# Optimization experiments

Measured on AMD Instinct MI355X. Metric: run time of the kernel, lower is better.

Reference implementation:

```python
import jax, jax.numpy as jnp
import numpy as np

S = 64        # state_dim
M = 16        # message_dim
H = 128       # hidden_unit_message_dim
HR = 128      # hidden_unit_readout_dim
NSTEPS = 10
N_NODES = 10000
N_FACTORS = 40000


def setup_inputs() -> dict:
    rng = np.random.default_rng(0)
    n, F = N_NODES, N_FACTORS
    # random undirected factor pairs (u, v) with u < v
    u = rng.integers(0, n - 1, F)
    v = rng.integers(u + 1, n)
    # var->factor directed edges: (u, i) and (v, i) for factor i
    v2f_src = np.stack([u, v], 1).ravel().astype(np.int32)          # [E]
    v2f_dst = np.repeat(np.arange(F), 2).astype(np.int32)           # [E]
    b = rng.normal(size=n).astype(np.float32)
    Juv = rng.normal(size=F).astype(np.float32)
    Jvu = rng.normal(size=F).astype(np.float32)
    feat_u = np.stack([b[u], b[v], Juv, Jvu], 1)
    feat_v = np.stack([b[v], b[u], Juv, Jvu], 1)
    feat = np.stack([feat_u, feat_v], 1).reshape(-1, 4).astype(np.float32)  # [E,4]
    p = lambda *s: (0.1 * rng.normal(size=s)).astype(np.float32)
    z = lambda *s: np.zeros(s, np.float32)
    inp = {
        'v2f_src': jnp.asarray(v2f_src), 'v2f_dst': jnp.asarray(v2f_dst),
        'f2v_src': jnp.asarray(v2f_dst), 'f2v_dst': jnp.asarray(v2f_src),
        'feat_v2f': jnp.asarray(feat), 'feat_f2v': jnp.asarray(feat),
        'n_nodes': n, 'n_factors': F,
        'Qw': jnp.asarray(p(4, M * M)), 'Qb': jnp.asarray(z(M * M)),
        'mp1_w1': jnp.asarray(p(2 * S, H)), 'mp1_b1': jnp.asarray(z(H)),
        'mp1_w2': jnp.asarray(p(H, H)), 'mp1_b2': jnp.asarray(z(H)),
        'mp1_w3': jnp.asarray(p(H, M)), 'mp1_b3': jnp.asarray(z(M)),
        'mp2_w1': jnp.asarray(p(2 * S, H)), 'mp2_b1': jnp.asarray(z(H)),
        'mp2_w2': jnp.asarray(p(H, H)), 'mp2_b2': jnp.asarray(z(H)),
        'mp2_w3': jnp.asarray(p(H, M)), 'mp2_b3': jnp.asarray(z(M)),
        'g1_wih': jnp.asarray(p(M, 3 * S)), 'g1_whh': jnp.asarray(p(S, 3 * S)),
        'g1_bih': jnp.asarray(z(3 * S)), 'g1_bhh': jnp.asarray(z(3 * S)),
        'g2_wih': jnp.asarray(p(M, 3 * S)), 'g2_whh': jnp.asarray(p(S, 3 * S)),
        'g2_bih': jnp.asarray(z(3 * S)), 'g2_bhh': jnp.asarray(z(3 * S)),
        'ro_w1': jnp.asarray(p(S, HR)), 'ro_b1': jnp.asarray(z(HR)),
        'ro_w2': jnp.asarray(p(HR, HR)), 'ro_b2': jnp.asarray(z(HR)),
        'ro_w3': jnp.asarray(p(HR, 2)), 'ro_b3': jnp.asarray(z(2)),
    }
    return inp


def _mlp(x, w1, b1, w2, b2, w3, b3):
    h = jax.nn.relu(x @ w1 + b1)
    h = jax.nn.relu(h @ w2 + b2)
    return h @ w3 + b3


def _gru(x, h, wih, whh, bih, bhh):
    # torch.nn.GRUCell gate order: r, z, n
    gi = x @ wih + bih
    gh = h @ whh + bhh
    ir, iz, inn = jnp.split(gi, 3, axis=-1)
    hr, hz, hn = jnp.split(gh, 3, axis=-1)
    r = jax.nn.sigmoid(ir + hr)
    zg = jax.nn.sigmoid(iz + hz)
    ng = jnp.tanh(inn + r * hn)
    return (1.0 - zg) * ng + zg * h


def reference(v2f_src, v2f_dst, f2v_src, f2v_dst, feat_v2f, feat_f2v,
              n_nodes, n_factors, Qw, Qb,
              mp1_w1, mp1_b1, mp1_w2, mp1_b2, mp1_w3, mp1_b3,
              mp2_w1, mp2_b1, mp2_w2, mp2_b2, mp2_w3, mp2_b3,
              g1_wih, g1_whh, g1_bih, g1_bhh,
              g2_wih, g2_whh, g2_bih, g2_bhh,
              ro_w1, ro_b1, ro_w2, ro_b2, ro_w3, ro_b3):
    var_h = jnp.zeros((n_nodes, S), feat_v2f.dtype)
    fac_h = jnp.zeros((n_factors, S), feat_v2f.dtype)
    # per-edge transform matrices are the same every step; hoist out of the loop
    q1 = (feat_v2f @ Qw + Qb).reshape(-1, M, M)  # [E, M, M]
    q2 = (feat_f2v @ Qw + Qb).reshape(-1, M, M)
    for _ in range(NSTEPS):
        # var -> factor
        x = jnp.concatenate([var_h[v2f_src], fac_h[v2f_dst]], axis=-1)  # [E, 2S]
        m = _mlp(x, mp1_w1, mp1_b1, mp1_w2, mp1_b2, mp1_w3, mp1_b3)    # [E, M]
        m = jnp.einsum('eij,ej->ei', q1, m)
        fac_msg = jax.ops.segment_sum(m, v2f_dst, num_segments=n_factors)
        fac_h = _gru(fac_msg, fac_h, g1_wih, g1_whh, g1_bih, g1_bhh)
        # factor -> var
        x = jnp.concatenate([fac_h[f2v_src], var_h[f2v_dst]], axis=-1)
        m = _mlp(x, mp2_w1, mp2_b1, mp2_w2, mp2_b2, mp2_w3, mp2_b3)
        m = jnp.einsum('eij,ej->ei', q2, m)
        var_msg = jax.ops.segment_sum(m, f2v_dst, num_segments=n_nodes)
        var_h = _gru(var_msg, var_h, g2_wih, g2_whh, g2_bih, g2_bhh)
    out = _mlp(var_h, ro_w1, ro_b1, ro_w2, ro_b2, ro_w3, ro_b3)  # [n_nodes, 2]
    return jax.nn.softmax(out, axis=1)
```

## Files before the change

### kernel.cpp

```cpp
#include <hip/hip_runtime.h>

#define NSTEPS 10

typedef __attribute__((ext_vector_type(8))) short bf16x8;
typedef __attribute__((ext_vector_type(4))) short bf16x4;
typedef __attribute__((ext_vector_type(4))) float f32x4;

__device__ __forceinline__ float sigmoidf_(float x) { return 1.0f / (1.0f + __expf(-x)); }
__device__ __forceinline__ float tanh_fast(float x) {
  const float e = __expf(2.f * x);
  return 1.f - 2.f / (e + 1.f);
}

__device__ __forceinline__ short bf16_(float x) {
  union { float f; unsigned u; } c; c.f = x;
  unsigned r = (c.u + 0x7FFFu + ((c.u >> 16) & 1u)) >> 16;
  return (short)r;
}
__device__ __forceinline__ unsigned pk2_(float a, float b) {
  union { float f; unsigned u; } ca, cb; ca.f = a; cb.f = b;
  return __builtin_amdgcn_perm(cb.u + 0x8000u, ca.u + 0x8000u, 0x07060302u);
}
__device__ __forceinline__ short pk1_(float a) {
  union { float f; unsigned u; } c; c.f = a;
  return (short)((c.u + 0x8000u) >> 16);
}
__device__ __forceinline__ float lo_(unsigned u) { union { unsigned u; float f; } c; c.u = u << 16; return c.f; }
__device__ __forceinline__ float hi_(unsigned u) { union { unsigned u; float f; } c; c.u = u & 0xffff0000u; return c.f; }

__device__ __forceinline__ f32x4 mfma_16x16x32(bf16x8 a, bf16x8 b, f32x4 c) {
  return __builtin_amdgcn_mfma_f32_16x16x32_bf16(a, b, c, 0, 0, 0);
}

struct PackJob { const float* src; int N; int KS; int nchunks; };
struct PackArgs {
  PackJob jb[10];
  const float* Qw; const float* Qb;
  const float* g1wih; const float* g1whh;
  const float* g2wih; const float* g2whh;
};

__global__ __launch_bounds__(256) void k_pack(PackArgs a, short* __restrict__ out, int total) {
  const int g = blockIdx.x * 256 + threadIdx.x;
  if (g >= total) return;
  int c = g >> 9;
  const int r = g & 511;
  const int j = r & 7, n = (r >> 3) & 15, q = (r >> 7) & 3;
  const int kq = q * 8 + j;
  float val = 0.f;
  bool done = false;
  #pragma unroll
  for (int ji = 0; ji < 10; ++ji) {
    if (!done && c < a.jb[ji].nchunks) {
      const int ks = c % a.jb[ji].KS;
      const int nt = c / a.jb[ji].KS;
      const int k = ks * 32 + kq;
      val = a.jb[ji].src[(size_t)k * a.jb[ji].N + nt * 16 + n];
      done = true;
    }
    if (!done) c -= a.jb[ji].nchunks;
  }
  if (!done) {
    if (c < 5) {
      val = 0.f;
      if (kq < 16) val = (c < 4) ? a.Qw[c * 256 + n * 16 + kq] : a.Qb[n * 16 + kq];
    } else {
      c -= 5;
      const float* wih = (c < 48) ? a.g1wih : a.g2wih;
      const float* whh = (c < 48) ? a.g1whh : a.g2whh;
      if (c >= 48) c -= 48;
      const int nt = c / 3, ks = c % 3;
      const int k = ks * 32 + kq;
      const int ng = nt * 16 + n;
      const int gate = ng >> 6, s = ng & 63;
      val = 0.f;
      if (gate == 0) {
        if (k < 16) val = wih[k * 192 + s];
        else if (k < 80) val = whh[(k - 16) * 192 + s];
      } else if (gate == 1) {
        if (k < 16) val = wih[k * 192 + 64 + s];
        else if (k < 80) val = whh[(k - 16) * 192 + 64 + s];
      } else if (gate == 2) {
        if (k < 16) val = wih[k * 192 + 128 + s];
      } else {
        if (k >= 16 && k < 80) val = whh[(k - 16) * 192 + 128 + s];
      }
    }
  }
  out[g] = bf16_(val);
}

__global__ __launch_bounds__(256) void k_dense2(
    const float* __restrict__ X0, const short* __restrict__ W0, short* __restrict__ C0,
    int rows0, int g0,
    const float* __restrict__ X1, const short* __restrict__ W1, short* __restrict__ C1,
    int rows1, float* __restrict__ zeroPtr,
    const float* __restrict__ gruMsg, float* __restrict__ gruH,
    const short* __restrict__ gruW,
    const float* __restrict__ gbih, const float* __restrict__ gbhh)
{
  constexpr int KS = 2, K = 64, STR = K + 8;
  __shared__ short Xs[64 * STR];
  __shared__ short SA[64 * 104];
  const int t = threadIdx.x, lane = t & 63, wave = t >> 6;
  const int m = lane & 15, quad = lane >> 4;

  const float* X; const short* Wf; short* C; int rows, rbase;
  const bool job0 = (int)blockIdx.x < g0;
  if (job0) {
    X = X0; Wf = W0; C = C0; rows = rows0; rbase = blockIdx.x * 64;
  } else {
    X = X1; Wf = W1; C = C1; rows = rows1; rbase = ((int)blockIdx.x - g0) * 64;
    if (zeroPtr) {
      const int zr = rbase + (t >> 2);
      if (zr < rows1) {
        f32x4 z = {0.f, 0.f, 0.f, 0.f};
        *(f32x4*)(zeroPtr + (size_t)zr * 16 + (t & 3) * 4) = z;
      }
    }
  }

  bf16x8 b[2][KS];
  #pragma unroll
  for (int nt2 = 0; nt2 < 2; ++nt2)
    #pragma unroll
    for (int ks = 0; ks < KS; ++ks)
      b[nt2][ks] = ((const bf16x8*)Wf)[((wave * 2 + nt2) * KS + ks) * 64 + lane];

  if (job0 && gruMsg) {
    {
      const int r = t >> 2, q4 = t & 3, rg = rbase + r;
      #pragma unroll
      for (int i = 0; i < 6; ++i) {
        const int c = q4 * 4 + i * 16;
        f32x4 v = {0.f, 0.f, 0.f, 0.f};
        if (rg < rows) {
          if (c < 16)      v = *(const f32x4*)(gruMsg + (size_t)rg * 16 + c);
          else if (c < 80) v = *(const f32x4*)(gruH + (size_t)rg * 64 + (c - 16));
        }
        *(unsigned*)&SA[r * 104 + c]     = pk2_(v.x, v.y);
        *(unsigned*)&SA[r * 104 + c + 2] = pk2_(v.z, v.w);
      }
    }
    __syncthreads();
    f32x4 acc[16] = {};
    #pragma unroll
    for (int ks = 0; ks < 3; ++ks) {
      const bf16x8 a = *(const bf16x8*)&SA[(wave * 16 + m) * 104 + ks * 32 + quad * 8];
      #pragma unroll
      for (int nt = 0; nt < 16; ++nt)
        acc[nt] = mfma_16x16x32(a, ((const bf16x8*)gruW)[(nt * 3 + ks) * 64 + lane], acc[nt]);
    }
    #pragma unroll
    for (int nt = 0; nt < 4; ++nt) {
      const int s = nt * 16 + m;
      const float br  = gbih[s] + gbhh[s];
      const float bz  = gbih[64 + s] + gbhh[64 + s];
      const float bin = gbih[128 + s];
      const float bhn = gbhh[128 + s];
      #pragma unroll
      for (int reg = 0; reg < 4; ++reg) {
        const int lr = wave * 16 + quad * 4 + reg;
        const int rg = rbase + lr;
        short hv = 0;
        if (rg < rows) {
          const float ho = gruH[(size_t)rg * 64 + s];
          const float rr = sigmoidf_(acc[nt][reg] + br);
          const float zz = sigmoidf_(acc[4 + nt][reg] + bz);
          const float nn = tanh_fast(acc[8 + nt][reg] + bin + rr * (acc[12 + nt][reg] + bhn));
          const float hn = (1.f - zz) * nn + zz * ho;
          gruH[(size_t)rg * 64 + s] = hn;
          hv = pk1_(hn);
        }
        Xs[lr * STR + s] = hv;
      }
    }
    __syncthreads();
  } else {
    const int r = t >> 2, q4 = t & 3, rg = rbase + r;
    #pragma unroll
    for (int i = 0; i < K / 16; ++i) {
      const int cc = q4 * 4 + i * 16;
      f32x4 v = {0.f, 0.f, 0.f, 0.f};
      if (rg < rows) v = *(const f32x4*)(X + (size_t)rg * K + cc);
      *(unsigned*)&Xs[r * STR + cc]     = pk2_(v.x, v.y);
      *(unsigned*)&Xs[r * STR + cc + 2] = pk2_(v.z, v.w);
    }
    __syncthreads();
  }

  f32x4 acc[2][4] = {};
  #pragma unroll
  for (int ks = 0; ks < KS; ++ks) {
    bf16x8 afr[4];
    #pragma unroll
    for (int mt = 0; mt < 4; ++mt)
      afr[mt] = *(const bf16x8*)&Xs[(mt * 16 + m) * STR + ks * 32 + quad * 8];
    #pragma unroll
    for (int nt2 = 0; nt2 < 2; ++nt2)
      #pragma unroll
      for (int mt = 0; mt < 4; ++mt)
        acc[nt2][mt] = mfma_16x16x32(afr[mt], b[nt2][ks], acc[nt2][mt]);
  }

  #pragma unroll
  for (int nt2 = 0; nt2 < 2; ++nt2) {
    const int col = (wave * 2 + nt2) * 16 + m;
    #pragma unroll
    for (int mt = 0; mt < 4; ++mt)
      #pragma unroll
      for (int rr = 0; rr < 4; ++rr) {
        const int rg = rbase + mt * 16 + quad * 4 + rr;
        if (rg < rows) C[(size_t)rg * 128 + col] = pk1_(acc[nt2][mt][rr]);
      }
  }
}

template<bool PAIRED>
__global__ __launch_bounds__(256) void k_edge(
    const short* __restrict__ Pa, const short* __restrict__ Pb,
    const int* __restrict__ src, const int* __restrict__ dst,
    const float* __restrict__ feat,
    const float* __restrict__ b1, const float* __restrict__ b2,
    const float* __restrict__ b3,
    const short* __restrict__ w2f, const short* __restrict__ w3f,
    const short* __restrict__ qf,
    float* __restrict__ outMsg,
    float* __restrict__ facH, const short* __restrict__ gruW,
    const float* __restrict__ gbih, const float* __restrict__ gbhh,
    int E, int F)
{
  __shared__ short h1s[64 * 136];
  __shared__ short ms[64 * 40];
  __shared__ short AsG[32 * 104];
  __shared__ float feats[64 * 4];
  __shared__ int sidx[64], didx[64];

  const int t = threadIdx.x, lane = t & 63, wave = t >> 6;
  const int e0 = blockIdx.x * 64;
  const int f0 = e0 >> 1;

  if (t < 64) {
    const int eg = e0 + t;
    sidx[t] = (eg < E) ? src[eg] : 0;
    didx[t] = (eg < E) ? dst[eg] : 0;
  }
  {
    const int e = t >> 2, k = t & 3;
    const int eg = e0 + e;
    feats[e * 4 + k] = (eg < E) ? feat[(size_t)eg * 4 + k] : 0.f;
  }
  if (PAIRED) {
    const int hr = t >> 3, hc = (t & 7) * 8;
    const int f = f0 + hr;
    f32x4 a0 = {0.f,0.f,0.f,0.f}, a1 = {0.f,0.f,0.f,0.f};
    if (f < F) {
      a0 = *(const f32x4*)(facH + (size_t)f * 64 + hc);
      a1 = *(const f32x4*)(facH + (size_t)f * 64 + hc + 4);
    }
    uint4 o;
    o.x = pk2_(a0.x, a0.y); o.y = pk2_(a0.z, a0.w);
    o.z = pk2_(a1.x, a1.y); o.w = pk2_(a1.z, a1.w);
    *(uint4*)&AsG[hr * 104 + 16 + hc] = o;
    if (t < 64) {
      uint4 z = make_uint4(0u, 0u, 0u, 0u);
      *(uint4*)&AsG[(t >> 1) * 104 + 80 + (t & 1) * 8] = z;
    }
  }
  bf16x8 bw2[2][4];
  #pragma unroll
  for (int nt2 = 0; nt2 < 2; ++nt2)
    #pragma unroll
    for (int ks = 0; ks < 4; ++ks)
      bw2[nt2][ks] = ((const bf16x8*)w2f)[((wave * 2 + nt2) * 4 + ks) * 64 + lane];
  __syncthreads();

  {
    const int r = t >> 2, q4 = t & 3;
    const bool ok = (e0 + r) < E;
    const short* pa = Pa + (size_t)sidx[r] * 128;
    const short* pb = Pb + (size_t)didx[r] * 128;
    #pragma unroll
    for (int i = 0; i < 4; ++i) {
      const int col = (q4 + i * 4) * 8;
      uint4 o = make_uint4(0u, 0u, 0u, 0u);
      if (ok) {
        const uint4 ua = *(const uint4*)(pa + col);
        const uint4 ub = *(const uint4*)(pb + col);
        const f32x4 ba = *(const f32x4*)(b1 + col);
        const f32x4 bb = *(const f32x4*)(b1 + col + 4);
        o.x = pk2_(fmaxf(lo_(ua.x) + lo_(ub.x) + ba.x, 0.f),
                   fmaxf(hi_(ua.x) + hi_(ub.x) + ba.y, 0.f));
        o.y = pk2_(fmaxf(lo_(ua.y) + lo_(ub.y) + ba.z, 0.f),
                   fmaxf(hi_(ua.y) + hi_(ub.y) + ba.w, 0.f));
        o.z = pk2_(fmaxf(lo_(ua.z) + lo_(ub.z) + bb.x, 0.f),
                   fmaxf(hi_(ua.z) + hi_(ub.z) + bb.y, 0.f));
        o.w = pk2_(fmaxf(lo_(ua.w) + lo_(ub.w) + bb.z, 0.f),
                   fmaxf(hi_(ua.w) + hi_(ub.w) + bb.w, 0.f));
      }
      *(uint4*)&h1s[r * 136 + col] = o;
    }
  }
  __syncthreads();

  const int m = lane & 15, quad = lane >> 4;

  f32x4 acc2[2][4] = {};
  #pragma unroll
  for (int ks = 0; ks < 4; ++ks) {
    bf16x8 afr[4];
    #pragma unroll
    for (int mt = 0; mt < 4; ++mt)
      afr[mt] = *(const bf16x8*)&h1s[(mt * 16 + m) * 136 + ks * 32 + quad * 8];
    #pragma unroll
    for (int nt2 = 0; nt2 < 2; ++nt2)
      #pragma unroll
      for (int mt = 0; mt < 4; ++mt)
        acc2[nt2][mt] = mfma_16x16x32(afr[mt], bw2[nt2][ks], acc2[nt2][mt]);
  }
  __syncthreads();

  #pragma unroll
  for (int nt2 = 0; nt2 < 2; ++nt2) {
    const int col = (wave * 2 + nt2) * 16 + m;
    const float bv = b2[col];
    #pragma unroll
    for (int mt = 0; mt < 4; ++mt)
      #pragma unroll
      for (int rr = 0; rr < 4; ++rr)
        h1s[(mt * 16 + quad * 4 + rr) * 136 + col] =
            pk1_(fmaxf(acc2[nt2][mt][rr] + bv, 0.f));
  }
  bf16x8 bw3[4];
  #pragma unroll
  for (int ks = 0; ks < 4; ++ks) bw3[ks] = ((const bf16x8*)w3f)[ks * 64 + lane];
  bf16x8 bq[5];
  #pragma unroll
  for (int tq = 0; tq < 5; ++tq) bq[tq] = ((const bf16x8*)qf)[tq * 64 + lane];
  __syncthreads();

  f32x4 acc3 = {};
  #pragma unroll
  for (int ks = 0; ks < 4; ++ks) {
    const bf16x8 afr = *(const bf16x8*)&h1s[(wave * 16 + m) * 136 + ks * 32 + quad * 8];
    acc3 = mfma_16x16x32(afr, bw3[ks], acc3);
  }
  const float b3v = b3[m];
  #pragma unroll
  for (int rr = 0; rr < 4; ++rr) {
    const int row = wave * 16 + quad * 4 + rr;
    ms[row * 40 + m] = pk1_(acc3[rr] + b3v);
    ms[row * 40 + 16 + m] = 0;
  }
  __syncthreads();

  f32x4 accY[5] = {};
  {
    const bf16x8 afr = *(const bf16x8*)&ms[(wave * 16 + m) * 40 + quad * 8];
    #pragma unroll
    for (int tq = 0; tq < 5; ++tq) accY[tq] = mfma_16x16x32(afr, bq[tq], accY[tq]);
  }
  float mq[4];
  #pragma unroll
  for (int rr = 0; rr < 4; ++rr) {
    const int row = wave * 16 + quad * 4 + rr;
    const f32x4 f = *(const f32x4*)&feats[row * 4];
    mq[rr] = accY[4][rr] + f.x * accY[0][rr] + f.y * accY[1][rr]
                         + f.z * accY[2][rr] + f.w * accY[3][rr];
  }

  if (PAIRED) {
    {
      const int fl = wave * 8 + quad * 2;
      AsG[fl * 104 + m]       = pk1_(mq[0] + mq[1]);
      AsG[(fl + 1) * 104 + m] = pk1_(mq[2] + mq[3]);
    }
    __syncthreads();
    const int mt = wave >> 1, sh = wave & 1;
    f32x4 accG[8] = {};
    #pragma unroll
    for (int ks = 0; ks < 3; ++ks) {
      const bf16x8 a = *(const bf16x8*)&AsG[(mt * 16 + m) * 104 + ks * 32 + quad * 8];
      #pragma unroll
      for (int g = 0; g < 4; ++g)
        #pragma unroll
        for (int nt2 = 0; nt2 < 2; ++nt2) {
          const int nt = g * 4 + sh * 2 + nt2;
          accG[g * 2 + nt2] =
              mfma_16x16x32(a, ((const bf16x8*)gruW)[(nt * 3 + ks) * 64 + lane],
                            accG[g * 2 + nt2]);
        }
    }
    #pragma unroll
    for (int nt2 = 0; nt2 < 2; ++nt2) {
      const int s = sh * 32 + nt2 * 16 + m;
      const float br  = gbih[s] + gbhh[s];
      const float bz  = gbih[64 + s] + gbhh[64 + s];
      const float bin = gbih[128 + s];
      const float bhn = gbhh[128 + s];
      #pragma unroll
      for (int reg = 0; reg < 4; ++reg) {
        const int f = f0 + mt * 16 + quad * 4 + reg;
        if (f < F) {
          const float ho = facH[(size_t)f * 64 + s];
          const float rr = sigmoidf_(accG[nt2][reg] + br);
          const float zz = sigmoidf_(accG[2 + nt2][reg] + bz);
          const float nn = tanh_fast(accG[4 + nt2][reg] + bin +
                                     rr * (accG[6 + nt2][reg] + bhn));
          facH[(size_t)f * 64 + s] = (1.f - zz) * nn + zz * ho;
        }
      }
    }
  } else {
    #pragma unroll
    for (int rr = 0; rr < 4; ++rr) {
      const int erow = wave * 16 + quad * 4 + rr;
      if (e0 + erow < E)
        atomicAdd(outMsg + (size_t)didx[erow] * 16 + m, mq[rr]);
    }
  }
}

__global__ __launch_bounds__(256) void k_readout_f(
    const float* __restrict__ gruMsg, const float* __restrict__ gruH,
    const short* __restrict__ gruW,
    const float* __restrict__ gbih, const float* __restrict__ gbhh,
    const short* __restrict__ ro1f, const float* __restrict__ rob1,
    const short* __restrict__ ro2f, const float* __restrict__ rob2,
    const float* __restrict__ row3, const float* __restrict__ rob3,
    float* __restrict__ out, int rows)
{
  __shared__ short SA[64 * 104];
  __shared__ short SH[64 * 72];
  __shared__ short S1[64 * 136];
  __shared__ short S2[64 * 136];
  __shared__ float w3s[256];
  const int t = threadIdx.x, lane = t & 63, wave = t >> 6;
  const int m = lane & 15, quad = lane >> 4;
  const int rbase = blockIdx.x * 64;

  w3s[t] = row3[t];

  {
    const int r = t >> 2, q4 = t & 3, rg = rbase + r;
    #pragma unroll
    for (int i = 0; i < 6; ++i) {
      const int c = q4 * 4 + i * 16;
      f32x4 v = {0.f, 0.f, 0.f, 0.f};
      if (rg < rows) {
        if (c < 16)      v = *(const f32x4*)(gruMsg + (size_t)rg * 16 + c);
        else if (c < 80) v = *(const f32x4*)(gruH + (size_t)rg * 64 + (c - 16));
      }
      *(unsigned*)&SA[r * 104 + c]     = pk2_(v.x, v.y);
      *(unsigned*)&SA[r * 104 + c + 2] = pk2_(v.z, v.w);
    }
  }
  __syncthreads();
  {
    f32x4 acc[16] = {};
    #pragma unroll
    for (int ks = 0; ks < 3; ++ks) {
      const bf16x8 a = *(const bf16x8*)&SA[(wave * 16 + m) * 104 + ks * 32 + quad * 8];
      #pragma unroll
      for (int nt = 0; nt < 16; ++nt)
        acc[nt] = mfma_16x16x32(a, ((const bf16x8*)gruW)[(nt * 3 + ks) * 64 + lane], acc[nt]);
    }
    #pragma unroll
    for (int nt = 0; nt < 4; ++nt) {
      const int s = nt * 16 + m;
      const float br  = gbih[s] + gbhh[s];
      const float bz  = gbih[64 + s] + gbhh[64 + s];
      const float bin = gbih[128 + s];
      const float bhn = gbhh[128 + s];
      #pragma unroll
      for (int reg = 0; reg < 4; ++reg) {
        const int lr = wave * 16 + quad * 4 + reg;
        const int rg = rbase + lr;
        short hv = 0;
        if (rg < rows) {
          const float ho = gruH[(size_t)rg * 64 + s];
          const float rr = sigmoidf_(acc[nt][reg] + br);
          const float zz = sigmoidf_(acc[4 + nt][reg] + bz);
          const float nn = tanh_fast(acc[8 + nt][reg] + bin + rr * (acc[12 + nt][reg] + bhn));
          hv = pk1_((1.f - zz) * nn + zz * ho);
        }
        SH[lr * 72 + s] = hv;
      }
    }
  }
  __syncthreads();

  {
    f32x4 acc[2][4] = {};
    #pragma unroll
    for (int ks = 0; ks < 2; ++ks) {
      bf16x8 afr[4];
      #pragma unroll
      for (int mt = 0; mt < 4; ++mt)
        afr[mt] = *(const bf16x8*)&SH[(mt * 16 + m) * 72 + ks * 32 + quad * 8];
      #pragma unroll
      for (int nt2 = 0; nt2 < 2; ++nt2) {
        const bf16x8 bb = ((const bf16x8*)ro1f)[((wave * 2 + nt2) * 2 + ks) * 64 + lane];
        #pragma unroll
        for (int mt = 0; mt < 4; ++mt)
          acc[nt2][mt] = mfma_16x16x32(afr[mt], bb, acc[nt2][mt]);
      }
    }
    #pragma unroll
    for (int nt2 = 0; nt2 < 2; ++nt2) {
      const int col = (wave * 2 + nt2) * 16 + m;
      const float bv = rob1[col];
      #pragma unroll
      for (int mt = 0; mt < 4; ++mt)
        #pragma unroll
        for (int rr = 0; rr < 4; ++rr)
          S1[(mt * 16 + quad * 4 + rr) * 136 + col] =
              pk1_(fmaxf(acc[nt2][mt][rr] + bv, 0.f));
    }
  }
  __syncthreads();

  {
    f32x4 acc[2][4] = {};
    #pragma unroll
    for (int ks = 0; ks < 4; ++ks) {
      bf16x8 afr[4];
      #pragma unroll
      for (int mt = 0; mt < 4; ++mt)
        afr[mt] = *(const bf16x8*)&S1[(mt * 16 + m) * 136 + ks * 32 + quad * 8];
      #pragma unroll
      for (int nt2 = 0; nt2 < 2; ++nt2) {
        const bf16x8 bb = ((const bf16x8*)ro2f)[((wave * 2 + nt2) * 4 + ks) * 64 + lane];
        #pragma unroll
        for (int mt = 0; mt < 4; ++mt)
          acc[nt2][mt] = mfma_16x16x32(afr[mt], bb, acc[nt2][mt]);
      }
    }
    #pragma unroll
    for (int nt2 = 0; nt2 < 2; ++nt2) {
      const int col = (wave * 2 + nt2) * 16 + m;
      const float bv = rob2[col];
      #pragma unroll
      for (int mt = 0; mt < 4; ++mt)
        #pragma unroll
        for (int rr = 0; rr < 4; ++rr)
          S2[(mt * 16 + quad * 4 + rr) * 136 + col] =
              pk1_(fmaxf(acc[nt2][mt][rr] + bv, 0.f));
    }
  }
  __syncthreads();

  if (t < 64) {
    const int rg = rbase + t;
    if (rg < rows) {
      float l0 = rob3[0], l1 = rob3[1];
      #pragma unroll 8
      for (int k = 0; k < 128; k += 2) {
        const unsigned u = *(const unsigned*)&S2[t * 136 + k];
        const float x0 = lo_(u), x1 = hi_(u);
        l0 = fmaf(x0, w3s[k * 2 + 0], l0);
        l1 = fmaf(x0, w3s[k * 2 + 1], l1);
        l0 = fmaf(x1, w3s[k * 2 + 2], l0);
        l1 = fmaf(x1, w3s[k * 2 + 3], l1);
      }
      const float mx = fmaxf(l0, l1);
      const float e0 = __expf(l0 - mx), e1 = __expf(l1 - mx);
      const float inv = 1.f / (e0 + e1);
      out[(size_t)rg * 2 + 0] = e0 * inv;
      out[(size_t)rg * 2 + 1] = e1 * inv;
    }
  }
}

extern "C" void kernel_launch(void* const* d_in, const int* in_sizes, int n_in,
                              void* d_out, int out_size, void* d_ws, size_t ws_size,
                              hipStream_t stream)
{
  const int*   v2f_src  = (const int*)d_in[0];
  const int*   v2f_dst  = (const int*)d_in[1];
  const int*   f2v_src  = (const int*)d_in[2];
  const int*   f2v_dst  = (const int*)d_in[3];
  const float* feat_v2f = (const float*)d_in[4];
  const float* feat_f2v = (const float*)d_in[5];
  const float* Qw    = (const float*)d_in[8];
  const float* Qb    = (const float*)d_in[9];
  const float* m1w1  = (const float*)d_in[10];
  const float* m1b1  = (const float*)d_in[11];
  const float* m1w2  = (const float*)d_in[12];
  const float* m1b2  = (const float*)d_in[13];
  const float* m1w3  = (const float*)d_in[14];
  const float* m1b3  = (const float*)d_in[15];
  const float* m2w1  = (const float*)d_in[16];
  const float* m2b1  = (const float*)d_in[17];
  const float* m2w2  = (const float*)d_in[18];
  const float* m2b2  = (const float*)d_in[19];
  const float* m2w3  = (const float*)d_in[20];
  const float* m2b3  = (const float*)d_in[21];
  const float* g1wih = (const float*)d_in[22];
  const float* g1whh = (const float*)d_in[23];
  const float* g1bih = (const float*)d_in[24];
  const float* g1bhh = (const float*)d_in[25];
  const float* g2wih = (const float*)d_in[26];
  const float* g2whh = (const float*)d_in[27];
  const float* g2bih = (const float*)d_in[28];
  const float* g2bhh = (const float*)d_in[29];
  const float* row1  = (const float*)d_in[30];
  const float* rob1  = (const float*)d_in[31];
  const float* row2  = (const float*)d_in[32];
  const float* rob2  = (const float*)d_in[33];
  const float* row3  = (const float*)d_in[34];
  const float* rob3  = (const float*)d_in[35];

  const int E = in_sizes[0];
  const int N = out_size / 2;
  const int F = E / 2;

  float* ws    = (float*)d_ws;
  float* var_h = ws;
  float* fac_h = var_h + (size_t)N * 64;
  float* msgV  = fac_h + (size_t)F * 64;
  short* Abuf  = (short*)(msgV + (size_t)N * 16);
  short* Bbuf  = Abuf + (size_t)F * 128;
  short* wb    = Bbuf + (size_t)F * 128;

  const int C_W2A = 0,  C_W2B = 32, C_W3A = 64, C_W3B = 68;
  const int C_W1AS = 72, C_W1AD = 88, C_W1BS = 104, C_W1BD = 120;
  const int C_RO1 = 136, C_RO2 = 152, C_Q = 184, C_G1 = 189, C_G2 = 237;
  const int TOTAL_CHUNKS = 285;

  short* PB_w2a  = wb + C_W2A  * 512;
  short* PB_w2b  = wb + C_W2B  * 512;
  short* PB_w3a  = wb + C_W3A  * 512;
  short* PB_w3b  = wb + C_W3B  * 512;
  short* PB_w1as = wb + C_W1AS * 512;
  short* PB_w1ad = wb + C_W1AD * 512;
  short* PB_w1bs = wb + C_W1BS * 512;
  short* PB_w1bd = wb + C_W1BD * 512;
  short* PB_ro1  = wb + C_RO1  * 512;
  short* PB_ro2  = wb + C_RO2  * 512;
  short* PB_q    = wb + C_Q    * 512;
  short* PB_g1   = wb + C_G1   * 512;
  short* PB_g2   = wb + C_G2   * 512;

  hipMemsetAsync(var_h, 0, (size_t)N * 64 * sizeof(float), stream);
  hipMemsetAsync(fac_h, 0, (size_t)F * 64 * sizeof(float), stream);

  PackArgs pa;
  pa.jb[0] = {m1w2,            128, 4, 32};
  pa.jb[1] = {m2w2,            128, 4, 32};
  pa.jb[2] = {m1w3,             16, 4,  4};
  pa.jb[3] = {m2w3,             16, 4,  4};
  pa.jb[4] = {m1w1,            128, 2, 16};
  pa.jb[5] = {m1w1 + 64 * 128, 128, 2, 16};
  pa.jb[6] = {m2w1,            128, 2, 16};
  pa.jb[7] = {m2w1 + 64 * 128, 128, 2, 16};
  pa.jb[8] = {row1,            128, 2, 16};
  pa.jb[9] = {row2,            128, 4, 32};
  pa.Qw = Qw; pa.Qb = Qb;
  pa.g1wih = g1wih; pa.g1whh = g1whh;
  pa.g2wih = g2wih; pa.g2whh = g2whh;
  const int packTotal = TOTAL_CHUNKS * 512;
  k_pack<<<(packTotal + 255) / 256, 256, 0, stream>>>(pa, wb, packTotal);

  const int gN = (N + 63) / 64;
  const int gF = (F + 63) / 64;
  const int gE = (E + 63) / 64;

  for (int step = 0; step < NSTEPS; ++step) {
    k_dense2<<<gN + gF, 256, 0, stream>>>(
        var_h, PB_w1as, Abuf, N, gN,
        fac_h, PB_w1ad, Bbuf, F, nullptr,
        step ? msgV : nullptr, var_h, PB_g2, g2bih, g2bhh);
    k_edge<true><<<gE, 256, 0, stream>>>(
        Abuf, Bbuf, v2f_src, v2f_dst, feat_v2f, m1b1, m1b2, m1b3,
        PB_w2a, PB_w3a, PB_q, nullptr, fac_h, PB_g1, g1bih, g1bhh, E, F);
    k_dense2<<<gF + gN, 256, 0, stream>>>(
        fac_h, PB_w1bs, Abuf, F, gF,
        var_h, PB_w1bd, Bbuf, N, msgV,
        nullptr, nullptr, nullptr, nullptr, nullptr);
    k_edge<false><<<gE, 256, 0, stream>>>(
        Abuf, Bbuf, f2v_src, f2v_dst, feat_f2v, m2b1, m2b2, m2b3,
        PB_w2b, PB_w3b, PB_q, msgV, nullptr, nullptr, nullptr, nullptr, E, F);
  }

  k_readout_f<<<gN, 256, 0, stream>>>(
      msgV, var_h, PB_g2, g2bih, g2bhh,
      PB_ro1, rob1, PB_ro2, rob2, row3, rob3, (float*)d_out, N);
}
```

Baseline: 717.1 us.

## Fuse per-step pipeline into two kernels exploiting factor-local edge structure

Replaces four kernels per step (two dense projections, two edge kernels) with two. Phase A runs the variable GRU and projects var_h through both variable-side W1 halves at once into Abuf and Bbuf. Phase B handles the var->factor edges, factor GRU, and factor->var edges in a single block. It relies on each factor owning two consecutive edges, so the factor-side projections are computed in shared memory instead of being staged in global buffers. This removes launches and global round-trips of the factor-side intermediates, at the cost of a heavier block with more shared memory and assumptions about the edge layout.

Result: no change. 706.1 us (-1.5%).

```diff
diff --git a/kernel.cpp b/kernel.cpp
--- a/kernel.cpp
+++ b/kernel.cpp
@@ -3,7 +3,6 @@
 #define NSTEPS 10
 
 typedef __attribute__((ext_vector_type(8))) short bf16x8;
-typedef __attribute__((ext_vector_type(4))) short bf16x4;
 typedef __attribute__((ext_vector_type(4))) float f32x4;
 
 __device__ __forceinline__ float sigmoidf_(float x) { return 1.0f / (1.0f + __expf(-x)); }
@@ -11,7 +10,6 @@
   const float e = __expf(2.f * x);
   return 1.f - 2.f / (e + 1.f);
 }
-
 __device__ __forceinline__ short bf16_(float x) {
   union { float f; unsigned u; } c; c.f = x;
   unsigned r = (c.u + 0x7FFFu + ((c.u >> 16) & 1u)) >> 16;
@@ -31,6 +29,20 @@
 __device__ __forceinline__ f32x4 mfma_16x16x32(bf16x8 a, bf16x8 b, f32x4 c) {
   return __builtin_amdgcn_mfma_f32_16x16x32_bf16(a, b, c, 0, 0, 0);
 }
+
+#define C_W2A   0
+#define C_W2B   32
+#define C_W3A   64
+#define C_W3B   68
+#define C_ACOMB 72
+#define C_W1AD  104
+#define C_W1BS  120
+#define C_RO1   136
+#define C_RO2   152
+#define C_Q     184
+#define C_G1    189
+#define C_G2    237
+#define TOTAL_CHUNKS 285
 
 struct PackJob { const float* src; int N; int KS; int nchunks; };
 struct PackArgs {
@@ -40,9 +52,7 @@
   const float* g2wih; const float* g2whh;
 };
 
-__global__ __launch_bounds__(256) void k_pack(PackArgs a, short* __restrict__ out, int total) {
-  const int g = blockIdx.x * 256 + threadIdx.x;
-  if (g >= total) return;
+__device__ __forceinline__ float pack_val(const PackArgs& a, int g) {
   int c = g >> 9;
   const int r = g & 511;
   const int j = r & 7, n = (r >> 3) & 15, q = (r >> 7) & 3;
@@ -87,176 +97,235 @@
       }
     }
   }
-  out[g] = bf16_(val);
-}
-
-__global__ __launch_bounds__(256) void k_dense2(
-    const float* __restrict__ X0, const short* __restrict__ W0, short* __restrict__ C0,
-    int rows0, int g0,
-    const float* __restrict__ X1, const short* __restrict__ W1, short* __restrict__ C1,
-    int rows1, float* __restrict__ zeroPtr,
-    const float* __restrict__ gruMsg, float* __restrict__ gruH,
-    const short* __restrict__ gruW,
-    const float* __restrict__ gbih, const float* __restrict__ gbhh)
+  return val;
+}
+
+__global__ __launch_bounds__(256) void k_pack(PackArgs a, short* __restrict__ out, int total) {
+  const int g = blockIdx.x * 256 + threadIdx.x;
+  if (g < total) out[g] = bf16_(pack_val(a, g));
+}
+
+__device__ __forceinline__ void edge_tail(
+    const short* wb, int cw2, int cw3,
+    const float* b2, const float* b3,
+    short* h1s, short* ms, const float* feats,
+    int lane, int wave, int m, int quad, float* mq)
 {
-  constexpr int KS = 2, K = 64, STR = K + 8;
-  __shared__ short Xs[64 * STR];
+  f32x4 acc2[2][4] = {};
+  #pragma unroll
+  for (int ks = 0; ks < 4; ++ks) {
+    bf16x8 afr[4];
+    #pragma unroll
+    for (int mt = 0; mt < 4; ++mt)
+      afr[mt] = *(const bf16x8*)&h1s[(mt * 16 + m) * 136 + ks * 32 + quad * 8];
+    #pragma unroll
+    for (int nt2 = 0; nt2 < 2; ++nt2) {
+      const bf16x8 bfr = ((const bf16x8*)(wb + cw2))[((wave * 2 + nt2) * 4 + ks) * 64 + lane];
+      #pragma unroll
+      for (int mt = 0; mt < 4; ++mt)
+        acc2[nt2][mt] = mfma_16x16x32(afr[mt], bfr, acc2[nt2][mt]);
+    }
+  }
+  __syncthreads();
+  #pragma unroll
+  for (int nt2 = 0; nt2 < 2; ++nt2) {
+    const int col = (wave * 2 + nt2) * 16 + m;
+    const float bv = b2[col];
+    #pragma unroll
+    for (int mt = 0; mt < 4; ++mt)
+      #pragma unroll
+      for (int rr = 0; rr < 4; ++rr)
+        h1s[(mt * 16 + quad * 4 + rr) * 136 + col] =
+            pk1_(fmaxf(acc2[nt2][mt][rr] + bv, 0.f));
+  }
+  __syncthreads();
+  f32x4 acc3 = {};
+  #pragma unroll
+  for (int ks = 0; ks < 4; ++ks) {
+    const bf16x8 afr = *(const bf16x8*)&h1s[(wave * 16 + m) * 136 + ks * 32 + quad * 8];
+    acc3 = mfma_16x16x32(afr, ((const bf16x8*)(wb + cw3))[ks * 64 + lane], acc3);
+  }
+  const float b3v = b3[m];
+  #pragma unroll
+  for (int rr = 0; rr < 4; ++rr) {
+    const int row = wave * 16 + quad * 4 + rr;
+    ms[row * 40 + m] = pk1_(acc3[rr] + b3v);
+    ms[row * 40 + 16 + m] = 0;
+  }
+  __syncthreads();
+  f32x4 accY[5] = {};
+  {
+    const bf16x8 afr = *(const bf16x8*)&ms[(wave * 16 + m) * 40 + quad * 8];
+    #pragma unroll
+    for (int tq = 0; tq < 5; ++tq)
+      accY[tq] = mfma_16x16x32(afr, ((const bf16x8*)(wb + C_Q * 512))[tq * 64 + lane], accY[tq]);
+  }
+  #pragma unroll
+  for (int rr = 0; rr < 4; ++rr) {
+    const int row = wave * 16 + quad * 4 + rr;
+    const f32x4 f = *(const f32x4*)&feats[row * 4];
+    mq[rr] = accY[4][rr] + f.x * accY[0][rr] + f.y * accY[1][rr]
+                         + f.z * accY[2][rr] + f.w * accY[3][rr];
+  }
+}
+
+__device__ __forceinline__ void var_gru_tile(
+    const short* wb, const float* gbih, const float* gbhh,
+    const short* SA, float* gruH, short* outTile, int outStr,
+    int rbase, int Nn, int lane, int wave, int m, int quad, bool writeH)
+{
+  f32x4 acc[16] = {};
+  #pragma unroll
+  for (int ks = 0; ks < 3; ++ks) {
+    const bf16x8 av = *(const bf16x8*)&SA[(wave * 16 + m) * 104 + ks * 32 + quad * 8];
+    #pragma unroll
+    for (int nt = 0; nt < 16; ++nt)
+      acc[nt] = mfma_16x16x32(av, ((const bf16x8*)(wb + C_G2 * 512))[(nt * 3 + ks) * 64 + lane], acc[nt]);
+  }
+  #pragma unroll
+  for (int nt = 0; nt < 4; ++nt) {
+    const int s = nt * 16 + m;
+    const float br  = gbih[s] + gbhh[s];
+    const float bz  = gbih[64 + s] + gbhh[64 + s];
+    const float bin = gbih[128 + s];
+    const float bhn = gbhh[128 + s];
+    #pragma unroll
+    for (int reg = 0; reg < 4; ++reg) {
+      const int lr = wave * 16 + quad * 4 + reg, rg = rbase + lr;
+      short hv = 0;
+      if (rg < Nn) {
+        const float ho = gruH[(size_t)rg * 64 + s];
+        const float rr = sigmoidf_(acc[nt][reg] + br);
+        const float zz = sigmoidf_(acc[4 + nt][reg] + bz);
+        const float nn = tanh_fast(acc[8 + nt][reg] + bin + rr * (acc[12 + nt][reg] + bhn));
+        const float hn = (1.f - zz) * nn + zz * ho;
+        if (writeH) gruH[(size_t)rg * 64 + s] = hn;
+        hv = pk1_(hn);
+      }
+      outTile[lr * outStr + s] = hv;
+    }
+  }
+}
+
+__global__ __launch_bounds__(256) void k_phaseA(
+    const float* __restrict__ msgIn, float* __restrict__ msgZero,
+    float* __restrict__ var_h,
+    short* __restrict__ Abuf, short* __restrict__ Bbuf,
+    const short* __restrict__ wb,
+    const float* __restrict__ gbih, const float* __restrict__ gbhh, int N)
+{
   __shared__ short SA[64 * 104];
+  __shared__ short Xs[64 * 72];
   const int t = threadIdx.x, lane = t & 63, wave = t >> 6;
   const int m = lane & 15, quad = lane >> 4;
-
-  const float* X; const short* Wf; short* C; int rows, rbase;
-  const bool job0 = (int)blockIdx.x < g0;
-  if (job0) {
-    X = X0; Wf = W0; C = C0; rows = rows0; rbase = blockIdx.x * 64;
-  } else {
-    X = X1; Wf = W1; C = C1; rows = rows1; rbase = ((int)blockIdx.x - g0) * 64;
-    if (zeroPtr) {
-      const int zr = rbase + (t >> 2);
-      if (zr < rows1) {
-        f32x4 z = {0.f, 0.f, 0.f, 0.f};
-        *(f32x4*)(zeroPtr + (size_t)zr * 16 + (t & 3) * 4) = z;
-      }
-    }
-  }
-
-  bf16x8 b[2][KS];
-  #pragma unroll
-  for (int nt2 = 0; nt2 < 2; ++nt2)
-    #pragma unroll
-    for (int ks = 0; ks < KS; ++ks)
-      b[nt2][ks] = ((const bf16x8*)Wf)[((wave * 2 + nt2) * KS + ks) * 64 + lane];
-
-  if (job0 && gruMsg) {
+  const int rbase = blockIdx.x * 64;
+
+  if (msgIn) {
     {
       const int r = t >> 2, q4 = t & 3, rg = rbase + r;
       #pragma unroll
       for (int i = 0; i < 6; ++i) {
         const int c = q4 * 4 + i * 16;
         f32x4 v = {0.f, 0.f, 0.f, 0.f};
-        if (rg < rows) {
-          if (c < 16)      v = *(const f32x4*)(gruMsg + (size_t)rg * 16 + c);
-          else if (c < 80) v = *(const f32x4*)(gruH + (size_t)rg * 64 + (c - 16));
+        if (rg < N) {
+          if (c < 16)      v = *(const f32x4*)(msgIn + (size_t)rg * 16 + c);
+          else if (c < 80) v = *(const f32x4*)(var_h + (size_t)rg * 64 + (c - 16));
         }
         *(unsigned*)&SA[r * 104 + c]     = pk2_(v.x, v.y);
         *(unsigned*)&SA[r * 104 + c + 2] = pk2_(v.z, v.w);
       }
+      if (rbase + r < N) {
+        f32x4 z = {0.f, 0.f, 0.f, 0.f};
+        *(f32x4*)(msgZero + (size_t)(rbase + r) * 16 + q4 * 4) = z;
+      }
     }
     __syncthreads();
-    f32x4 acc[16] = {};
-    #pragma unroll
-    for (int ks = 0; ks < 3; ++ks) {
-      const bf16x8 a = *(const bf16x8*)&SA[(wave * 16 + m) * 104 + ks * 32 + quad * 8];
-      #pragma unroll
-      for (int nt = 0; nt < 16; ++nt)
-        acc[nt] = mfma_16x16x32(a, ((const bf16x8*)gruW)[(nt * 3 + ks) * 64 + lane], acc[nt]);
-    }
-    #pragma unroll
-    for (int nt = 0; nt < 4; ++nt) {
-      const int s = nt * 16 + m;
-      const float br  = gbih[s] + gbhh[s];
-      const float bz  = gbih[64 + s] + gbhh[64 + s];
-      const float bin = gbih[128 + s];
-      const float bhn = gbhh[128 + s];
-      #pragma unroll
-      for (int reg = 0; reg < 4; ++reg) {
-        const int lr = wave * 16 + quad * 4 + reg;
-        const int rg = rbase + lr;
-        short hv = 0;
-        if (rg < rows) {
-          const float ho = gruH[(size_t)rg * 64 + s];
-          const float rr = sigmoidf_(acc[nt][reg] + br);
-          const float zz = sigmoidf_(acc[4 + nt][reg] + bz);
-          const float nn = tanh_fast(acc[8 + nt][reg] + bin + rr * (acc[12 + nt][reg] + bhn));
-          const float hn = (1.f - zz) * nn + zz * ho;
-          gruH[(size_t)rg * 64 + s] = hn;
-          hv = pk1_(hn);
-        }
-        Xs[lr * STR + s] = hv;
-      }
-    }
+    var_gru_tile(wb, gbih, gbhh, SA, var_h, Xs, 72,
+                 rbase, N, lane, wave, m, quad, true);
     __syncthreads();
   } else {
     const int r = t >> 2, q4 = t & 3, rg = rbase + r;
     #pragma unroll
-    for (int i = 0; i < K / 16; ++i) {
+    for (int i = 0; i < 4; ++i) {
       const int cc = q4 * 4 + i * 16;
       f32x4 v = {0.f, 0.f, 0.f, 0.f};
-      if (rg < rows) v = *(const f32x4*)(X + (size_t)rg * K + cc);
-      *(unsigned*)&Xs[r * STR + cc]     = pk2_(v.x, v.y);
-      *(unsigned*)&Xs[r * STR + cc + 2] = pk2_(v.z, v.w);
+      if (rg < N) v = *(const f32x4*)(var_h + (size_t)rg * 64 + cc);
+      *(unsigned*)&Xs[r * 72 + cc]     = pk2_(v.x, v.y);
+      *(unsigned*)&Xs[r * 72 + cc + 2] = pk2_(v.z, v.w);
     }
     __syncthreads();
   }
 
-  f32x4 acc[2][4] = {};
-  #pragma unroll
-  for (int ks = 0; ks < KS; ++ks) {
+  f32x4 acc[4][4] = {};
+  #pragma unroll
+  for (int ks = 0; ks < 2; ++ks) {
     bf16x8 afr[4];
     #pragma unroll
     for (int mt = 0; mt < 4; ++mt)
-      afr[mt] = *(const bf16x8*)&Xs[(mt * 16 + m) * STR + ks * 32 + quad * 8];
-    #pragma unroll
-    for (int nt2 = 0; nt2 < 2; ++nt2)
+      afr[mt] = *(const bf16x8*)&Xs[(mt * 16 + m) * 72 + ks * 32 + quad * 8];
+    #pragma unroll
+    for (int j = 0; j < 4; ++j) {
+      const bf16x8 bfr = ((const bf16x8*)(wb + C_ACOMB * 512))[((wave * 4 + j) * 2 + ks) * 64 + lane];
       #pragma unroll
       for (int mt = 0; mt < 4; ++mt)
-        acc[nt2][mt] = mfma_16x16x32(afr[mt], b[nt2][ks], acc[nt2][mt]);
-  }
-
-  #pragma unroll
-  for (int nt2 = 0; nt2 < 2; ++nt2) {
-    const int col = (wave * 2 + nt2) * 16 + m;
+        acc[j][mt] = mfma_16x16x32(afr[mt], bfr, acc[j][mt]);
+    }
+  }
+  #pragma unroll
+  for (int j = 0; j < 4; ++j) {
+    const int col = (wave * 4 + j) * 16 + m;
+    short* dst = (col < 128) ? Abuf : Bbuf;
+    const int c2 = col & 127;
     #pragma unroll
     for (int mt = 0; mt < 4; ++mt)
       #pragma unroll
-      for (int rr = 0; rr < 4; ++rr) {
-        const int rg = rbase + mt * 16 + quad * 4 + rr;
-        if (rg < rows) C[(size_t)rg * 128 + col] = pk1_(acc[nt2][mt][rr]);
-      }
-  }
-}
-
-template<bool PAIRED>
-__global__ __launch_bounds__(256) void k_edge(
-    const short* __restrict__ Pa, const short* __restrict__ Pb,
-    const int* __restrict__ src, const int* __restrict__ dst,
-    const float* __restrict__ feat,
-    const float* __restrict__ b1, const float* __restrict__ b2,
-    const float* __restrict__ b3,
-    const short* __restrict__ w2f, const short* __restrict__ w3f,
-    const short* __restrict__ qf,
-    float* __restrict__ outMsg,
-    float* __restrict__ facH, const short* __restrict__ gruW,
-    const float* __restrict__ gbih, const float* __restrict__ gbhh,
-    int E, int F)
+      for (int reg = 0; reg < 4; ++reg) {
+        const int rg = rbase + mt * 16 + quad * 4 + reg;
+        if (rg < N) dst[(size_t)rg * 128 + c2] = pk1_(acc[j][mt][reg]);
+      }
+  }
+}
+
+__global__ __launch_bounds__(256) void k_phaseB(
+    const short* __restrict__ Abuf, const short* __restrict__ Bbuf,
+    const int* __restrict__ v2f_src, const int* __restrict__ f2v_dst,
+    const float* __restrict__ featA, const float* __restrict__ featB,
+    const float* __restrict__ m1b1, const float* __restrict__ m1b2,
+    const float* __restrict__ m1b3,
+    const float* __restrict__ m2b1, const float* __restrict__ m2b2,
+    const float* __restrict__ m2b3,
+    const float* __restrict__ g1bih, const float* __restrict__ g1bhh,
+    const short* __restrict__ wb,
+    float* __restrict__ fac_h, float* __restrict__ msgV, int E, int F)
 {
+  __shared__ short AsG[32 * 104];
+  __shared__ short Ps[32 * 136];
   __shared__ short h1s[64 * 136];
   __shared__ short ms[64 * 40];
-  __shared__ short AsG[32 * 104];
+  __shared__ short Fs2[32 * 72];
   __shared__ float feats[64 * 4];
   __shared__ int sidx[64], didx[64];
 
   const int t = threadIdx.x, lane = t & 63, wave = t >> 6;
-  const int e0 = blockIdx.x * 64;
-  const int f0 = e0 >> 1;
+  const int m = lane & 15, quad = lane >> 4;
+  const int e0 = blockIdx.x * 64, f0 = blockIdx.x * 32;
 
   if (t < 64) {
     const int eg = e0 + t;
-    sidx[t] = (eg < E) ? src[eg] : 0;
-    didx[t] = (eg < E) ? dst[eg] : 0;
-  }
-  {
-    const int e = t >> 2, k = t & 3;
-    const int eg = e0 + e;
-    feats[e * 4 + k] = (eg < E) ? feat[(size_t)eg * 4 + k] : 0.f;
-  }
-  if (PAIRED) {
+    sidx[t] = (eg < E) ? v2f_src[eg] : 0;
+    didx[t] = (eg < E) ? f2v_dst[eg] : 0;
+  }
+  {
+    const int e = t >> 2, k = t & 3, eg = e0 + e;
+    feats[e * 4 + k] = (eg < E) ? featA[(size_t)eg * 4 + k] : 0.f;
+  }
+  {
     const int hr = t >> 3, hc = (t & 7) * 8;
     const int f = f0 + hr;
     f32x4 a0 = {0.f,0.f,0.f,0.f}, a1 = {0.f,0.f,0.f,0.f};
     if (f < F) {
-      a0 = *(const f32x4*)(facH + (size_t)f * 64 + hc);
-      a1 = *(const f32x4*)(facH + (size_t)f * 64 + hc + 4);
+      a0 = *(const f32x4*)(fac_h + (size_t)f * 64 + hc);
+      a1 = *(const f32x4*)(fac_h + (size_t)f * 64 + hc + 4);
     }
     uint4 o;
     o.x = pk2_(a0.x, a0.y); o.y = pk2_(a0.z, a0.w);
@@ -267,19 +336,35 @@
       *(uint4*)&AsG[(t >> 1) * 104 + 80 + (t & 1) * 8] = z;
     }
   }
-  bf16x8 bw2[2][4];
-  #pragma unroll
-  for (int nt2 = 0; nt2 < 2; ++nt2)
-    #pragma unroll
-    for (int ks = 0; ks < 4; ++ks)
-      bw2[nt2][ks] = ((const bf16x8*)w2f)[((wave * 2 + nt2) * 4 + ks) * 64 + lane];
+  __syncthreads();
+
+  {
+    const int mt = wave & 1, ng = wave >> 1;
+    f32x4 pacc[4] = {};
+    #pragma unroll
+    for (int ks = 0; ks < 2; ++ks) {
+      const bf16x8 av = *(const bf16x8*)&AsG[(mt * 16 + m) * 104 + 16 + ks * 32 + quad * 8];
+      #pragma unroll
+      for (int j = 0; j < 4; ++j) {
+        const bf16x8 bfr = ((const bf16x8*)(wb + C_W1AD * 512))[((ng * 4 + j) * 2 + ks) * 64 + lane];
+        pacc[j] = mfma_16x16x32(av, bfr, pacc[j]);
+      }
+    }
+    #pragma unroll
+    for (int j = 0; j < 4; ++j) {
+      const int col = (ng * 4 + j) * 16 + m;
+      #pragma unroll
+      for (int reg = 0; reg < 4; ++reg)
+        Ps[(mt * 16 + quad * 4 + reg) * 136 + col] = pk1_(pacc[j][reg]);
+    }
+  }
   __syncthreads();
 
   {
     const int r = t >> 2, q4 = t & 3;
     const bool ok = (e0 + r) < E;
-    const short* pa = Pa + (size_t)sidx[r] * 128;
-    const short* pb = Pb + (size_t)didx[r] * 128;
+    const short* pa = Abuf + (size_t)sidx[r] * 128;
+    const short* pb = Ps + (r >> 1) * 136;
     #pragma unroll
     for (int i = 0; i < 4; ++i) {
       const int col = (q4 + i * 4) * 8;
@@ -287,8 +372,8 @@
       if (ok) {
         const uint4 ua = *(const uint4*)(pa + col);
         const uint4 ub = *(const uint4*)(pb + col);
-        const f32x4 ba = *(const f32x4*)(b1 + col);
-        const f32x4 bb = *(const f32x4*)(b1 + col + 4);
+        const f32x4 ba = *(const f32x4*)(m1b1 + col);
+        const f32x4 bb = *(const f32x4*)(m1b1 + col + 4);
         o.x = pk2_(fmaxf(lo_(ua.x) + lo_(ub.x) + ba.x, 0.f),
                    fmaxf(hi_(ua.x) + hi_(ub.x) + ba.y, 0.f));
         o.y = pk2_(fmaxf(lo_(ua.y) + lo_(ub.y) + ba.z, 0.f),
@@ -303,130 +388,130 @@
   }
   __syncthreads();
 
-  const int m = lane & 15, quad = lane >> 4;
-
-  f32x4 acc2[2][4] = {};
-  #pragma unroll
-  for (int ks = 0; ks < 4; ++ks) {
-    bf16x8 afr[4];
-    #pragma unroll
-    for (int mt = 0; mt < 4; ++mt)
-      afr[mt] = *(const bf16x8*)&h1s[(mt * 16 + m) * 136 + ks * 32 + quad * 8];
-    #pragma unroll
-    for (int nt2 = 0; nt2 < 2; ++nt2)
-      #pragma unroll
-      for (int mt = 0; mt < 4; ++mt)
-        acc2[nt2][mt] = mfma_16x16x32(afr[mt], bw2[nt2][ks], acc2[nt2][mt]);
-  }
-  __syncthreads();
-
-  #pragma unroll
-  for (int nt2 = 0; nt2 < 2; ++nt2) {
-    const int col = (wave * 2 + nt2) * 16 + m;
-    const float bv = b2[col];
-    #pragma unroll
-    for (int mt = 0; mt < 4; ++mt)
-      #pragma unroll
-      for (int rr = 0; rr < 4; ++rr)
-        h1s[(mt * 16 + quad * 4 + rr) * 136 + col] =
-            pk1_(fmaxf(acc2[nt2][mt][rr] + bv, 0.f));
-  }
-  bf16x8 bw3[4];
-  #pragma unroll
-  for (int ks = 0; ks < 4; ++ks) bw3[ks] = ((const bf16x8*)w3f)[ks * 64 + lane];
-  bf16x8 bq[5];
-  #pragma unroll
-  for (int tq = 0; tq < 5; ++tq) bq[tq] = ((const bf16x8*)qf)[tq * 64 + lane];
-  __syncthreads();
-
-  f32x4 acc3 = {};
-  #pragma unroll
-  for (int ks = 0; ks < 4; ++ks) {
-    const bf16x8 afr = *(const bf16x8*)&h1s[(wave * 16 + m) * 136 + ks * 32 + quad * 8];
-    acc3 = mfma_16x16x32(afr, bw3[ks], acc3);
-  }
-  const float b3v = b3[m];
-  #pragma unroll
-  for (int rr = 0; rr < 4; ++rr) {
-    const int row = wave * 16 + quad * 4 + rr;
-    ms[row * 40 + m] = pk1_(acc3[rr] + b3v);
-    ms[row * 40 + 16 + m] = 0;
-  }
-  __syncthreads();
-
-  f32x4 accY[5] = {};
-  {
-    const bf16x8 afr = *(const bf16x8*)&ms[(wave * 16 + m) * 40 + quad * 8];
-    #pragma unroll
-    for (int tq = 0; tq < 5; ++tq) accY[tq] = mfma_16x16x32(afr, bq[tq], accY[tq]);
-  }
   float mq[4];
-  #pragma unroll
-  for (int rr = 0; rr < 4; ++rr) {
-    const int row = wave * 16 + quad * 4 + rr;
-    const f32x4 f = *(const f32x4*)&feats[row * 4];
-    mq[rr] = accY[4][rr] + f.x * accY[0][rr] + f.y * accY[1][rr]
-                         + f.z * accY[2][rr] + f.w * accY[3][rr];
-  }
-
-  if (PAIRED) {
-    {
-      const int fl = wave * 8 + quad * 2;
-      AsG[fl * 104 + m]       = pk1_(mq[0] + mq[1]);
-      AsG[(fl + 1) * 104 + m] = pk1_(mq[2] + mq[3]);
-    }
-    __syncthreads();
-    const int mt = wave >> 1, sh = wave & 1;
+  edge_tail(wb, C_W2A * 512, C_W3A * 512, m1b2, m1b3,
+            h1s, ms, feats, lane, wave, m, quad, mq);
+  {
+    const int fl = wave * 8 + quad * 2;
+    AsG[fl * 104 + m]       = pk1_(mq[0] + mq[1]);
+    AsG[(fl + 1) * 104 + m] = pk1_(mq[2] + mq[3]);
+  }
+  __syncthreads();
+
+  {
+    const int mtg = wave >> 1, sh = wave & 1;
     f32x4 accG[8] = {};
     #pragma unroll
     for (int ks = 0; ks < 3; ++ks) {
-      const bf16x8 a = *(const bf16x8*)&AsG[(mt * 16 + m) * 104 + ks * 32 + quad * 8];
+      const bf16x8 av = *(const bf16x8*)&AsG[(mtg * 16 + m) * 104 + ks * 32 + quad * 8];
       #pragma unroll
       for (int g = 0; g < 4; ++g)
         #pragma unroll
         for (int nt2 = 0; nt2 < 2; ++nt2) {
           const int nt = g * 4 + sh * 2 + nt2;
-          accG[g * 2 + nt2] =
-              mfma_16x16x32(a, ((const bf16x8*)gruW)[(nt * 3 + ks) * 64 + lane],
-                            accG[g * 2 + nt2]);
+          accG[g * 2 + nt2] = mfma_16x16x32(
+              av, ((const bf16x8*)(wb + C_G1 * 512))[(nt * 3 + ks) * 64 + lane],
+              accG[g * 2 + nt2]);
         }
     }
     #pragma unroll
     for (int nt2 = 0; nt2 < 2; ++nt2) {
       const int s = sh * 32 + nt2 * 16 + m;
-      const float br  = gbih[s] + gbhh[s];
-      const float bz  = gbih[64 + s] + gbhh[64 + s];
-      const float bin = gbih[128 + s];
-      const float bhn = gbhh[128 + s];
+      const float br  = g1bih[s] + g1bhh[s];
+      const float bz  = g1bih[64 + s] + g1bhh[64 + s];
+      const float bin = g1bih[128 + s];
+      const float bhn = g1bhh[128 + s];
       #pragma unroll
       for (int reg = 0; reg < 4; ++reg) {
-        const int f = f0 + mt * 16 + quad * 4 + reg;
+        const int lr = mtg * 16 + quad * 4 + reg;
+        const int f = f0 + lr;
+        short hv = 0;
         if (f < F) {
-          const float ho = facH[(size_t)f * 64 + s];
+          const float ho = fac_h[(size_t)f * 64 + s];
           const float rr = sigmoidf_(accG[nt2][reg] + br);
           const float zz = sigmoidf_(accG[2 + nt2][reg] + bz);
           const float nn = tanh_fast(accG[4 + nt2][reg] + bin +
                                      rr * (accG[6 + nt2][reg] + bhn));
-          facH[(size_t)f * 64 + s] = (1.f - zz) * nn + zz * ho;
+          const float hn = (1.f - zz) * nn + zz * ho;
+          fac_h[(size_t)f * 64 + s] = hn;
+          hv = pk1_(hn);
         }
-      }
-    }
-  } else {
-    #pragma unroll
-    for (int rr = 0; rr < 4; ++rr) {
-      const int erow = wave * 16 + quad * 4 + rr;
-      if (e0 + erow < E)
-        atomicAdd(outMsg + (size_t)didx[erow] * 16 + m, mq[rr]);
-    }
+        Fs2[lr * 72 + s] = hv;
+      }
+    }
+  }
+  {
+    const int e = t >> 2, k = t & 3, eg = e0 + e;
+    feats[e * 4 + k] = (eg < E) ? featB[(size_t)eg * 4 + k] : 0.f;
+  }
+  __syncthreads();
+
+  {
+    const int mt = wave & 1, ng = wave >> 1;
+    f32x4 pacc[4] = {};
+    #pragma unroll
+    for (int ks = 0; ks < 2; ++ks) {
+      const bf16x8 av = *(const bf16x8*)&Fs2[(mt * 16 + m) * 72 + ks * 32 + quad * 8];
+      #pragma unroll
+      for (int j = 0; j < 4; ++j) {
+        const bf16x8 bfr = ((const bf16x8*)(wb + C_W1BS * 512))[((ng * 4 + j) * 2 + ks) * 64 + lane];
+        pacc[j] = mfma_16x16x32(av, bfr, pacc[j]);
+      }
+    }
+    #pragma unroll
+    for (int j = 0; j < 4; ++j) {
+      const int col = (ng * 4 + j) * 16 + m;
+      #pragma unroll
+      for (int reg = 0; reg < 4; ++reg)
+        Ps[(mt * 16 + quad * 4 + reg) * 136 + col] = pk1_(pacc[j][reg]);
+    }
+  }
+  __syncthreads();
+
+  {
+    const int r = t >> 2, q4 = t & 3;
+    const bool ok = (e0 + r) < E;
+    const short* pa = Ps + (r >> 1) * 136;
+    const short* pb = Bbuf + (size_t)didx[r] * 128;
+    #pragma unroll
+    for (int i = 0; i < 4; ++i) {
+      const int col = (q4 + i * 4) * 8;
+      uint4 o = make_uint4(0u, 0u, 0u, 0u);
+      if (ok) {
+        const uint4 ua = *(const uint4*)(pa + col);
+        const uint4 ub = *(const uint4*)(pb + col);
+        const f32x4 ba = *(const f32x4*)(m2b1 + col);
+        const f32x4 bb = *(const f32x4*)(m2b1 + col + 4);
+        o.x = pk2_(fmaxf(lo_(ua.x) + lo_(ub.x) + ba.x, 0.f),
+                   fmaxf(hi_(ua.x) + hi_(ub.x) + ba.y, 0.f));
+        o.y = pk2_(fmaxf(lo_(ua.y) + lo_(ub.y) + ba.z, 0.f),
+                   fmaxf(hi_(ua.y) + hi_(ub.y) + ba.w, 0.f));
+        o.z = pk2_(fmaxf(lo_(ua.z) + lo_(ub.z) + bb.x, 0.f),
+                   fmaxf(hi_(ua.z) + hi_(ub.z) + bb.y, 0.f));
+        o.w = pk2_(fmaxf(lo_(ua.w) + lo_(ub.w) + bb.z, 0.f),
+                   fmaxf(hi_(ua.w) + hi_(ub.w) + bb.w, 0.f));
+      }
+      *(uint4*)&h1s[r * 136 + col] = o;
+    }
+  }
+  __syncthreads();
+
+  float mq2[4];
+  edge_tail(wb, C_W2B * 512, C_W3B * 512, m2b2, m2b3,
+            h1s, ms, feats, lane, wave, m, quad, mq2);
+  #pragma unroll
+  for (int rr = 0; rr < 4; ++rr) {
+    const int erow = wave * 16 + quad * 4 + rr;
+    if (e0 + erow < E)
+      atomicAdd(msgV + (size_t)didx[erow] * 16 + m, mq2[rr]);
   }
 }
 
 __global__ __launch_bounds__(256) void k_readout_f(
     const float* __restrict__ gruMsg, const float* __restrict__ gruH,
-    const short* __restrict__ gruW,
+    const short* __restrict__ wb,
     const float* __restrict__ gbih, const float* __restrict__ gbhh,
-    const short* __restrict__ ro1f, const float* __restrict__ rob1,
-    const short* __restrict__ ro2f, const float* __restrict__ rob2,
+    const float* __restrict__ rob1, const float* __restrict__ rob2,
     const float* __restrict__ row3, const float* __restrict__ rob3,
     float* __restrict__ out, int rows)
 {
@@ -440,7 +525,6 @@
   const int rbase = blockIdx.x * 64;
 
   w3s[t] = row3[t];
-
   {
     const int r = t >> 2, q4 = t & 3, rg = rbase + r;
     #pragma unroll
@@ -456,40 +540,9 @@
     }
   }
   __syncthreads();
-  {
-    f32x4 acc[16] = {};
-    #pragma unroll
-    for (int ks = 0; ks < 3; ++ks) {
-      const bf16x8 a = *(const bf16x8*)&SA[(wave * 16 + m) * 104 + ks * 32 + quad * 8];
-      #pragma unroll
-      for (int nt = 0; nt < 16; ++nt)
-        acc[nt] = mfma_16x16x32(a, ((const bf16x8*)gruW)[(nt * 3 + ks) * 64 + lane], acc[nt]);
-    }
-    #pragma unroll
-    for (int nt = 0; nt < 4; ++nt) {
-      const int s = nt * 16 + m;
-      const float br  = gbih[s] + gbhh[s];
-      const float bz  = gbih[64 + s] + gbhh[64 + s];
-      const float bin = gbih[128 + s];
-      const float bhn = gbhh[128 + s];
-      #pragma unroll
-      for (int reg = 0; reg < 4; ++reg) {
-        const int lr = wave * 16 + quad * 4 + reg;
-        const int rg = rbase + lr;
-        short hv = 0;
-        if (rg < rows) {
-          const float ho = gruH[(size_t)rg * 64 + s];
-          const float rr = sigmoidf_(acc[nt][reg] + br);
-          const float zz = sigmoidf_(acc[4 + nt][reg] + bz);
-          const float nn = tanh_fast(acc[8 + nt][reg] + bin + rr * (acc[12 + nt][reg] + bhn));
-          hv = pk1_((1.f - zz) * nn + zz * ho);
-        }
-        SH[lr * 72 + s] = hv;
-      }
-    }
-  }
-  __syncthreads();
-
+  var_gru_tile(wb, gbih, gbhh, SA, (float*)gruH, SH, 72,
+               rbase, rows, lane, wave, m, quad, false);
+  __syncthreads();
   {
     f32x4 acc[2][4] = {};
     #pragma unroll
@@ -500,10 +553,10 @@
         afr[mt] = *(const bf16x8*)&SH[(mt * 16 + m) * 72 + ks * 32 + quad * 8];
       #pragma unroll
       for (int nt2 = 0; nt2 < 2; ++nt2) {
-        const bf16x8 bb = ((const bf16x8*)ro1f)[((wave * 2 + nt2) * 2 + ks) * 64 + lane];
+        const bf16x8 bfr = ((const bf16x8*)(wb + C_RO1 * 512))[((wave * 2 + nt2) * 2 + ks) * 64 + lane];
         #pragma unroll
         for (int mt = 0; mt < 4; ++mt)
-          acc[nt2][mt] = mfma_16x16x32(afr[mt], bb, acc[nt2][mt]);
+          acc[nt2][mt] = mfma_16x16x32(afr[mt], bfr, acc[nt2][mt]);
       }
     }
     #pragma unroll
@@ -519,7 +572,6 @@
     }
   }
   __syncthreads();
-
   {
     f32x4 acc[2][4] = {};
     #pragma unroll
@@ -530,10 +582,10 @@
         afr[mt] = *(const bf16x8*)&S1[(mt * 16 + m) * 136 + ks * 32 + quad * 8];
       #pragma unroll
       for (int nt2 = 0; nt2 < 2; ++nt2) {
-        const bf16x8 bb = ((const bf16x8*)ro2f)[((wave * 2 + nt2) * 4 + ks) * 64 + lane];
+        const bf16x8 bfr = ((const bf16x8*)(wb + C_RO2 * 512))[((wave * 2 + nt2) * 4 + ks) * 64 + lane];
         #pragma unroll
         for (int mt = 0; mt < 4; ++mt)
-          acc[nt2][mt] = mfma_16x16x32(afr[mt], bb, acc[nt2][mt]);
+          acc[nt2][mt] = mfma_16x16x32(afr[mt], bfr, acc[nt2][mt]);
       }
     }
     #pragma unroll
@@ -549,7 +601,6 @@
     }
   }
   __syncthreads();
-
   if (t < 64) {
     const int rg = rbase + t;
     if (rg < rows) {
@@ -577,8 +628,6 @@
                               hipStream_t stream)
 {
   const int*   v2f_src  = (const int*)d_in[0];
-  const int*   v2f_dst  = (const int*)d_in[1];
-  const int*   f2v_src  = (const int*)d_in[2];
   const int*   f2v_dst  = (const int*)d_in[3];
   const float* feat_v2f = (const float*)d_in[4];
   const float* feat_f2v = (const float*)d_in[5];
@@ -615,75 +664,47 @@
   const int N = out_size / 2;
   const int F = E / 2;
 
-  float* ws    = (float*)d_ws;
-  float* var_h = ws;
+  float* wsf   = (float*)d_ws;
+  float* var_h = wsf;
   float* fac_h = var_h + (size_t)N * 64;
   float* msgV  = fac_h + (size_t)F * 64;
   short* Abuf  = (short*)(msgV + (size_t)N * 16);
-  short* Bbuf  = Abuf + (size_t)F * 128;
-  short* wb    = Bbuf + (size_t)F * 128;
-
-  const int C_W2A = 0,  C_W2B = 32, C_W3A = 64, C_W3B = 68;
-  const int C_W1AS = 72, C_W1AD = 88, C_W1BS = 104, C_W1BD = 120;
-  const int C_RO1 = 136, C_RO2 = 152, C_Q = 184, C_G1 = 189, C_G2 = 237;
-  const int TOTAL_CHUNKS = 285;
-
-  short* PB_w2a  = wb + C_W2A  * 512;
-  short* PB_w2b  = wb + C_W2B  * 512;
-  short* PB_w3a  = wb + C_W3A  * 512;
-  short* PB_w3b  = wb + C_W3B  * 512;
-  short* PB_w1as = wb + C_W1AS * 512;
-  short* PB_w1ad = wb + C_W1AD * 512;
-  short* PB_w1bs = wb + C_W1BS * 512;
-  short* PB_w1bd = wb + C_W1BD * 512;
-  short* PB_ro1  = wb + C_RO1  * 512;
-  short* PB_ro2  = wb + C_RO2  * 512;
-  short* PB_q    = wb + C_Q    * 512;
-  short* PB_g1   = wb + C_G1   * 512;
-  short* PB_g2   = wb + C_G2   * 512;
-
-  hipMemsetAsync(var_h, 0, (size_t)N * 64 * sizeof(float), stream);
-  hipMemsetAsync(fac_h, 0, (size_t)F * 64 * sizeof(float), stream);
-
-  PackArgs pa;
-  pa.jb[0] = {m1w2,            128, 4, 32};
-  pa.jb[1] = {m2w2,            128, 4, 32};
-  pa.jb[2] = {m1w3,             16, 4,  4};
-  pa.jb[3] = {m2w3,             16, 4,  4};
-  pa.jb[4] = {m1w1,            128, 2, 16};
-  pa.jb[5] = {m1w1 + 64 * 128, 128, 2, 16};
-  pa.jb[6] = {m2w1,            128, 2, 16};
-  pa.jb[7] = {m2w1 + 64 * 128, 128, 2, 16};
-  pa.jb[8] = {row1,            128, 2, 16};
-  pa.jb[9] = {row2,            128, 4, 32};
-  pa.Qw = Qw; pa.Qb = Qb;
-  pa.g1wih = g1wih; pa.g1whh = g1whh;
-  pa.g2wih = g2wih; pa.g2whh = g2whh;
+  short* Bbuf  = Abuf + (size_t)N * 128;
+  short* wb    = Bbuf + (size_t)N * 128;
+
+  hipMemsetAsync(var_h, 0,
+                 ((size_t)N * 64 + (size_t)F * 64 + (size_t)N * 16) * sizeof(float),
+                 stream);
+
+  PackArgs pk;
+  pk.jb[0] = {m1w2,            128, 4, 32};
+  pk.jb[1] = {m2w2,            128, 4, 32};
+  pk.jb[2] = {m1w3,             16, 4,  4};
+  pk.jb[3] = {m2w3,             16, 4,  4};
+  pk.jb[4] = {m1w1,            128, 2, 16};
+  pk.jb[5] = {m2w1 + 64 * 128, 128, 2, 16};
+  pk.jb[6] = {m1w1 + 64 * 128, 128, 2, 16};
+  pk.jb[7] = {m2w1,            128, 2, 16};
+  pk.jb[8] = {row1,            128, 2, 16};
+  pk.jb[9] = {row2,            128, 4, 32};
+  pk.Qw = Qw; pk.Qb = Qb;
+  pk.g1wih = g1wih; pk.g1whh = g1whh;
+  pk.g2wih = g2wih; pk.g2whh = g2whh;
   const int packTotal = TOTAL_CHUNKS * 512;
-  k_pack<<<(packTotal + 255) / 256, 256, 0, stream>>>(pa, wb, packTotal);
+  k_pack<<<(packTotal + 255) / 256, 256, 0, stream>>>(pk, wb, packTotal);
 
   const int gN = (N + 63) / 64;
-  const int gF = (F + 63) / 64;
   const int gE = (E + 63) / 64;
 
   for (int step = 0; step < NSTEPS; ++step) {
-    k_dense2<<<gN + gF, 256, 0, stream>>>(
-        var_h, PB_w1as, Abuf, N, gN,
-        fac_h, PB_w1ad, Bbuf, F, nullptr,
-        step ? msgV : nullptr, var_h, PB_g2, g2bih, g2bhh);
-    k_edge<true><<<gE, 256, 0, stream>>>(
-        Abuf, Bbuf, v2f_src, v2f_dst, feat_v2f, m1b1, m1b2, m1b3,
-        PB_w2a, PB_w3a, PB_q, nullptr, fac_h, PB_g1, g1bih, g1bhh, E, F);
-    k_dense2<<<gF + gN, 256, 0, stream>>>(
-        fac_h, PB_w1bs, Abuf, F, gF,
-        var_h, PB_w1bd, Bbuf, N, msgV,
-        nullptr, nullptr, nullptr, nullptr, nullptr);
-    k_edge<false><<<gE, 256, 0, stream>>>(
-        Abuf, Bbuf, f2v_src, f2v_dst, feat_f2v, m2b1, m2b2, m2b3,
-        PB_w2b, PB_w3b, PB_q, msgV, nullptr, nullptr, nullptr, nullptr, E, F);
+    k_phaseA<<<gN, 256, 0, stream>>>(
+        step ? msgV : nullptr, msgV, var_h, Abuf, Bbuf, wb, g2bih, g2bhh, N);
+    k_phaseB<<<gE, 256, 0, stream>>>(
+        Abuf, Bbuf, v2f_src, f2v_dst, feat_v2f, feat_f2v,
+        m1b1, m1b2, m1b3, m2b1, m2b2, m2b3, g1bih, g1bhh,
+        wb, fac_h, msgV, E, F);
   }
 
   k_readout_f<<<gN, 256, 0, stream>>>(
-      msgV, var_h, PB_g2, g2bih, g2bhh,
-      PB_ro1, rob1, PB_ro2, rob2, row3, rob3, (float*)d_out, N);
-}
+      msgV, var_h, wb, g2bih, g2bhh, rob1, rob2, row3, rob3, (float*)d_out, N);
+}
```
